# Performance work log

Hardware: AMD Instinct MI355X
Metric: run time of the kernel (lower is better)

Reference implementation:

```python
import jax, jax.numpy as jnp
import numpy as np

B, S, M, E, H = 4, 2048, 1024, 8, 4096
CAP = 2 * (B * S) // E  # GShard top-2 capacity = 2*s/e = 2048


def setup_inputs() -> dict:
    key = jax.random.key(0)
    k = jax.random.split(key, 6)
    sc = 0.02
    return {
        "x": jax.random.normal(k[0], (B, S, M), jnp.float32),
        "wg": jax.random.normal(k[1], (M, E), jnp.float32) * sc,
        "w1": jax.random.normal(k[2], (E, M, H), jnp.float32) * sc,
        "b1": jnp.zeros((E, H), jnp.float32),
        "w2": jax.random.normal(k[3], (E, H, M), jnp.float32) * sc,
        "b2": jnp.zeros((E, M), jnp.float32),
    }


def top2gating(logits, capacity):
    # Faithful GShard/fairscale top2gating: logits [s, e]
    s, e = logits.shape
    gates = jax.nn.softmax(logits, axis=-1)
    idx1 = jnp.argmax(gates, axis=1)
    mask1 = jax.nn.one_hot(idx1, e, dtype=jnp.float32)
    logits2 = jnp.where(mask1 > 0, -jnp.inf, logits)
    idx2 = jnp.argmax(logits2, axis=1)
    mask2 = jax.nn.one_hot(idx2, e, dtype=jnp.float32)
    # positions within each expert's buffer
    loc1 = jnp.cumsum(mask1, axis=0) - 1.0
    loc2 = jnp.cumsum(mask2, axis=0) - 1.0 + jnp.sum(mask1, axis=0, keepdims=True)
    # load-balancing aux loss (computed before capacity drop, per fairscale)
    me = jnp.mean(gates, axis=0)
    ce = jnp.mean(mask1, axis=0)
    l_aux = jnp.mean(me * ce) * (e * e)
    # drop tokens over capacity
    mask1 = mask1 * (loc1 < capacity)
    mask2 = mask2 * (loc2 < capacity)
    loc1_s = jnp.sum(loc1 * mask1, axis=1).astype(jnp.int32)
    loc2_s = jnp.sum(loc2 * mask2, axis=1).astype(jnp.int32)
    gates1 = jnp.sum(gates * mask1, axis=1)
    gates2 = jnp.sum(gates * mask2, axis=1)
    denom = jnp.maximum(gates1 + gates2, 1e-9)
    gates1 = gates1 / denom
    gates2 = gates2 / denom
    # dense [s, e, c] combine weights (as in the original einsum formulation)
    oh1 = jax.nn.one_hot(loc1_s, capacity, dtype=jnp.float32)
    oh2 = jax.nn.one_hot(loc2_s, capacity, dtype=jnp.float32)
    combine = (gates1[:, None] * mask1)[:, :, None] * oh1[:, None, :] \
            + (gates2[:, None] * mask2)[:, :, None] * oh2[:, None, :]
    dispatch = combine > 0
    return l_aux, combine, dispatch


def reference(x, wg, w1, b1, w2, b2):
    d_model = x.shape[2]
    xf = x.reshape(-1, d_model)                      # [s, m]
    logits = xf @ wg                                 # [s, e]
    l_aux, combine, dispatch = top2gating(logits, CAP)
    # dispatch: dense one-hot scatter, as in torch.einsum('sec,sm->ecm')
    disp = jnp.einsum('sec,sm->ecm', dispatch.astype(xf.dtype), xf)
    # per-expert FFN (Linear -> ReLU -> Linear), vectorized over experts
    h = jax.nn.relu(jnp.einsum('ecm,emh->ech', disp, w1) + b1[:, None, :])
    eo = jnp.einsum('ech,ehm->ecm', h, w2) + b2[:, None, :]
    # combine: torch.einsum('sec,ecm->sm')
    out = jnp.einsum('sec,ecm->sm', combine, eo)
    return out.reshape(x.shape), l_aux
```

## Files before the change

### kernel.cpp

```cpp
#include <hip/hip_runtime.h>
#include <stdint.h>

typedef unsigned short u16;
typedef __attribute__((ext_vector_type(8))) short bf16x8;
typedef __attribute__((ext_vector_type(4))) float f32x4;

#define TOKENS 8192
#define DM 1024
#define NE 8
#define DH 4096
#define CAP 2048

__device__ __forceinline__ u16 f2bf(float f) {
  unsigned int u = __float_as_uint(f);
  u = u + 0x7FFFu + ((u >> 16) & 1u);
  return (u16)(u >> 16);
}

__device__ __forceinline__ void gll16(const void* g, void* l) {
  __builtin_amdgcn_global_load_lds(
      (const __attribute__((address_space(1))) unsigned int*)g,
      (__attribute__((address_space(3))) unsigned int*)l, 16, 0, 0);
}

__global__ __launch_bounds__(256) void gating_kernel(
    const float* __restrict__ x, const float* __restrict__ wg,
    int* __restrict__ idx1, int* __restrict__ idx2,
    float* __restrict__ g1r, float* __restrict__ g2r, float* __restrict__ me) {
  __shared__ float gsh[4][8];
  int lane = threadIdx.x & 63;
  int w = threadIdx.x >> 6;
  int t = blockIdx.x * 4 + w;
  const float* xr = x + (size_t)t * DM;
  double acc[8];
#pragma unroll
  for (int e = 0; e < 8; ++e) acc[e] = 0.0;
#pragma unroll
  for (int it = 0; it < 4; ++it) {
    float4 xv = ((const float4*)xr)[it * 64 + lane];
    int base = (it * 64 + lane) * 4;
    const float* wr = wg + (size_t)base * 8;
    float xs[4] = {xv.x, xv.y, xv.z, xv.w};
#pragma unroll
    for (int j = 0; j < 4; ++j)
#pragma unroll
      for (int e = 0; e < 8; ++e) acc[e] += (double)xs[j] * (double)wr[j * 8 + e];
  }
#pragma unroll
  for (int off = 32; off > 0; off >>= 1)
#pragma unroll
    for (int e = 0; e < 8; ++e) acc[e] += __shfl_down(acc[e], off);
  if (lane == 0) {
    float l[8];
#pragma unroll
    for (int e = 0; e < 8; ++e) l[e] = (float)acc[e];
    int i1 = 0;
    float v1 = l[0];
#pragma unroll
    for (int e = 1; e < 8; ++e)
      if (l[e] > v1) { v1 = l[e]; i1 = e; }
    int i2 = -1;
    float v2 = -3.4e38f;
#pragma unroll
    for (int e = 0; e < 8; ++e)
      if (e != i1 && l[e] > v2) { v2 = l[e]; i2 = e; }
    float s = 0.f;
    float p[8];
#pragma unroll
    for (int e = 0; e < 8; ++e) { p[e] = expf(l[e] - v1); s += p[e]; }
    float inv = 1.f / s;
    idx1[t] = i1;
    idx2[t] = i2;
    g1r[t] = inv;
    g2r[t] = expf(v2 - v1) * inv;
#pragma unroll
    for (int e = 0; e < 8; ++e) gsh[w][e] = p[e] * inv;
  }
  __syncthreads();
  if (threadIdx.x < 8) {
    int e = threadIdx.x;
    atomicAdd(&me[e], gsh[0][e] + gsh[1][e] + gsh[2][e] + gsh[3][e]);
  }
}

__global__ __launch_bounds__(1024) void scan_kernel(
    const int* __restrict__ idx1, const int* __restrict__ idx2,
    const float* __restrict__ g1r, const float* __restrict__ g2r,
    const float* __restrict__ me,
    int* __restrict__ slot1, int* __restrict__ slot2,
    float* __restrict__ g1n, float* __restrict__ g2n,
    int* __restrict__ slot2tok, float* __restrict__ laux) {
  __shared__ u16 c[16][1024];
  __shared__ u16 csum[16][32];
  __shared__ int tot[16];
  int tid = threadIdx.x;
  int i1[8], i2[8];
#pragma unroll
  for (int ctr = 0; ctr < 16; ++ctr) c[ctr][tid] = 0;
#pragma unroll
  for (int j = 0; j < 8; ++j) {
    int t = tid * 8 + j;
    i1[j] = idx1[t];
    i2[j] = idx2[t];
    c[i1[j]][tid]++;
    c[8 + i2[j]][tid]++;
  }
  __syncthreads();
  if (tid < 512) {
    int ctr = tid >> 5, ch = tid & 31;
    int s = 0;
#pragma unroll
    for (int i = 0; i < 32; ++i) s += c[ctr][ch * 32 + i];
    csum[ctr][ch] = (u16)s;
  }
  __syncthreads();
  if (tid < 16) {
    int run = 0;
#pragma unroll
    for (int ch = 0; ch < 32; ++ch) {
      int v = csum[tid][ch];
      csum[tid][ch] = (u16)run;
      run += v;
    }
    tot[tid] = run;
  }
  __syncthreads();
  if (tid < 512) {
    int ctr = tid >> 5, ch = tid & 31;
    int run = csum[ctr][ch];
#pragma unroll
    for (int i = 0; i < 32; ++i) {
      int v = c[ctr][ch * 32 + i];
      c[ctr][ch * 32 + i] = (u16)run;
      run += v;
    }
  }
  __syncthreads();
#pragma unroll
  for (int j = 0; j < 8; ++j) {
    int t = tid * 8 + j;
    int e1 = i1[j], e2 = i2[j];
    int L1 = c[e1][tid]++;
    int L2 = c[8 + e2][tid]++;
    L2 += tot[e2];
    bool kv1 = L1 < CAP, kv2 = L2 < CAP;
    float G1 = kv1 ? g1r[t] : 0.f;
    float G2 = kv2 ? g2r[t] : 0.f;
    float den = fmaxf(G1 + G2, 1e-9f);
    g1n[t] = G1 / den;
    g2n[t] = G2 / den;
    int s1 = kv1 ? (e1 * CAP + L1) : -1;
    int s2 = kv2 ? (e2 * CAP + L2) : -1;
    slot1[t] = s1;
    slot2[t] = s2;
    if (kv1) slot2tok[s1] = t;
    if (kv2) slot2tok[s2] = t;
  }
  if (tid == 0) {
    double a = 0.0;
    for (int e = 0; e < 8; ++e)
      a += ((double)me[e] / 8192.0) * ((double)tot[e] / 8192.0);
    laux[0] = (float)(a * 8.0);
  }
}

__global__ void transpose_kernel(const float* __restrict__ src, u16* __restrict__ dst,
                                 int R, int C) {
  __shared__ float tile[32][33];
  int tx = threadIdx.x, ty = threadIdx.y;
  int r0 = blockIdx.y * 32, c0 = blockIdx.x * 32;
  const float* s = src + (size_t)blockIdx.z * R * C;
  u16* d = dst + (size_t)blockIdx.z * R * C;
#pragma unroll
  for (int i = 0; i < 32; i += 8) tile[ty + i][tx] = s[(size_t)(r0 + ty + i) * C + c0 + tx];
  __syncthreads();
#pragma unroll
  for (int i = 0; i < 32; i += 8)
    d[(size_t)(c0 + ty + i) * R + r0 + tx] = f2bf(tile[tx][ty + i]);
}

__global__ void gather_kernel(const float* __restrict__ x, const int* __restrict__ slot2tok,
                              u16* __restrict__ xe) {
  int slot = blockIdx.y * CAP + blockIdx.x;
  int tok = slot2tok[slot];
  int tid = threadIdx.x;
  u16 o[8];
  if (tok >= 0) {
    const float4* xr = (const float4*)(x + (size_t)tok * DM);
    float4 a = xr[tid * 2], b = xr[tid * 2 + 1];
    o[0] = f2bf(a.x); o[1] = f2bf(a.y); o[2] = f2bf(a.z); o[3] = f2bf(a.w);
    o[4] = f2bf(b.x); o[5] = f2bf(b.y); o[6] = f2bf(b.z); o[7] = f2bf(b.w);
  } else {
#pragma unroll
    for (int j = 0; j < 8; ++j) o[j] = 0;
  }
  *(uint4*)(xe + (size_t)slot * DM + tid * 8) = *(const uint4*)o;
}

#define BAR()                              \
  {                                        \
    asm volatile("" ::: "memory");         \
    __builtin_amdgcn_s_barrier();          \
    asm volatile("" ::: "memory");         \
  }
#define VMCNT(n) asm volatile("s_waitcnt vmcnt(" #n ")" ::: "memory")

template <int RELU, int OUTBF16>
__global__ __launch_bounds__(512, 2) void gemm_kernel(
    const u16* __restrict__ A, const u16* __restrict__ Bt,
    const float* __restrict__ bias, void* __restrict__ Cv,
    int MO, int NO, int K) {
  __shared__ __align__(16) u16 As[2][256 * 64];
  __shared__ __align__(16) u16 Bs[2][256 * 64];
  const int tid = threadIdx.x;
  const int lane = tid & 63, wid = tid >> 6;
  const int wm = wid >> 2, wn = wid & 3;

  const int gx = gridDim.x, gy = gridDim.y;
  const int nwg = gx * gy * gridDim.z;
  const int L = (blockIdx.z * gy + blockIdx.y) * gx + blockIdx.x;
  const int cpx = nwg >> 3;
  const int Ls = (L & 7) * cpx + (L >> 3);
  const int bx = Ls % gx;
  const int tq = Ls / gx;
  const int by = tq % gy;
  const int eb = tq / gy;

  const size_t Ks2 = (size_t)K * 2;
  const char* Ag = (const char*)(A + (size_t)eb * MO * K + (size_t)by * 256 * K);
  const char* Bg = (const char*)(Bt + (size_t)eb * NO * K + (size_t)bx * 256 * K);
  const int rl = tid >> 3;
  const int sb = ((tid & 7) * 16) ^ ((rl & 7) << 4);
  Ag += (size_t)rl * Ks2 + sb;
  Bg += (size_t)rl * Ks2 + sb;
  char* AsB = ((char*)As) + tid * 16;
  char* BsB = ((char*)Bs) + tid * 16;
  const u16* AsE = &As[0][0];
  const u16* BsE = &Bs[0][0];
  const int fr = lane & 15, kg8 = (lane >> 4) * 8;
  const int swz = (fr & 7) << 3;

#define STAGE_A(BUF_, REG_, KT_) \
  gll16(Ag + (size_t)((REG_)*64) * Ks2 + (size_t)(KT_)*128, AsB + (BUF_)*32768 + (REG_)*8192)
#define STAGE_B(BUF_, REG_, KT_) \
  gll16(Bg + (size_t)((REG_)*64) * Ks2 + (size_t)(KT_)*128, BsB + (BUF_)*32768 + (REG_)*8192)
#define LDA(BUF_, M_, K_) \
  (*(const bf16x8*)&AsE[(BUF_)*16384 + (wm * 128 + (M_)*16 + fr) * 64 + (((K_)*32 + kg8) ^ swz)])
#define LDB(BUF_, N_, K_) \
  (*(const bf16x8*)&BsE[(BUF_)*16384 + (wn * 64 + (N_)*16 + fr) * 64 + (((K_)*32 + kg8) ^ swz)])
#define MFMA_Q(MB_, NB_)                                                            \
  _Pragma("unroll") for (int k = 0; k < 2; ++k)                                     \
  _Pragma("unroll") for (int m = 0; m < 4; ++m)                                     \
  _Pragma("unroll") for (int n = 0; n < 2; ++n)                                     \
      acc[(MB_) + m][(NB_) + n] = __builtin_amdgcn_mfma_f32_16x16x32_bf16(          \
          areg[m][k], breg[(NB_) + n][k], acc[(MB_) + m][(NB_) + n], 0, 0, 0)

  f32x4 acc[8][4];
#pragma unroll
  for (int i = 0; i < 8; ++i)
#pragma unroll
    for (int j = 0; j < 4; ++j) acc[i][j] = {0.f, 0.f, 0.f, 0.f};
  bf16x8 areg[4][2], breg[4][2];

  const int NT = K >> 6;

#define TILE_STEP(CUR_, NXT_, ST_)                                                  \
  {                                                                                 \
                          \
    STAGE_A(NXT_, 0, ST_); STAGE_A(NXT_, 1, ST_);                                   \
    STAGE_A(NXT_, 2, ST_); STAGE_A(NXT_, 3, ST_);                                   \
    STAGE_B(NXT_, 0, ST_); STAGE_B(NXT_, 1, ST_);                                   \
    STAGE_B(NXT_, 2, ST_); STAGE_B(NXT_, 3, ST_);                                   \
                                   \
    _Pragma("unroll") for (int m = 0; m < 4; ++m) {                                 \
      areg[m][0] = LDA(CUR_, m, 0); areg[m][1] = LDA(CUR_, m, 1);                   \
    }                                                                               \
    _Pragma("unroll") for (int n = 0; n < 4; ++n) {                                 \
      breg[n][0] = LDB(CUR_, n, 0); breg[n][1] = LDB(CUR_, n, 1);                   \
    }                                                                               \
    __builtin_amdgcn_s_setprio(1);                                                  \
    MFMA_Q(0, 0); MFMA_Q(0, 2);                                                     \
    __builtin_amdgcn_s_setprio(0);                                                  \
                          \
    _Pragma("unroll") for (int m = 0; m < 4; ++m) {                                 \
      areg[m][0] = LDA(CUR_, 4 + m, 0); areg[m][1] = LDA(CUR_, 4 + m, 1);           \
    }                                                                               \
    __builtin_amdgcn_s_setprio(1);                                                  \
    MFMA_Q(4, 0); MFMA_Q(4, 2);                                                     \
    __builtin_amdgcn_s_setprio(0);                                                  \
    VMCNT(0);           \
    BAR();              \
  }

  STAGE_A(0, 0, 0); STAGE_A(0, 1, 0); STAGE_A(0, 2, 0); STAGE_A(0, 3, 0);
  STAGE_B(0, 0, 0); STAGE_B(0, 1, 0); STAGE_B(0, 2, 0); STAGE_B(0, 3, 0);
  VMCNT(0);
  BAR();

  for (int t = 0; t < NT; t += 2) {
    const int s1 = (t + 1 < NT) ? t + 1 : NT - 1;
    const int s2 = (t + 2 < NT) ? t + 2 : NT - 1;
    TILE_STEP(0, 1, s1);
    TILE_STEP(1, 0, s2);
  }

  const int row0 = by * 256 + wm * 128 + (kg8 >> 3) * 4;
  const int col0 = bx * 256 + wn * 64 + fr;
  const float* be = bias + (size_t)eb * NO;
  size_t cbase = (size_t)eb * MO * NO;
#pragma unroll
  for (int m = 0; m < 8; ++m) {
#pragma unroll
    for (int n = 0; n < 4; ++n) {
      int col = col0 + n * 16;
      float bv = be[col];
#pragma unroll
      for (int r = 0; r < 4; ++r) {
        int row = row0 + m * 16 + r;
        float v = acc[m][n][r] + bv;
        if (RELU) v = fmaxf(v, 0.f);
        if (OUTBF16)
          ((u16*)Cv)[cbase + (size_t)row * NO + col] = f2bf(v);
        else
          ((float*)Cv)[cbase + (size_t)row * NO + col] = v;
      }
    }
  }
#undef TILE_STEP
#undef STAGE_A
#undef STAGE_B
#undef LDA
#undef LDB
#undef MFMA_Q
}

__global__ void combine_kernel(const float* __restrict__ eo,
                               const float* __restrict__ g1n, const float* __restrict__ g2n,
                               const int* __restrict__ slot1, const int* __restrict__ slot2,
                               float* __restrict__ out) {
  int t = blockIdx.x, tid = threadIdx.x;
  float g1 = g1n[t], g2 = g2n[t];
  int s1 = slot1[t], s2 = slot2[t];
  float4 o = make_float4(0.f, 0.f, 0.f, 0.f);
  if (s1 >= 0) {
    float4 a = ((const float4*)(eo + (size_t)s1 * DM))[tid];
    o.x = g1 * a.x; o.y = g1 * a.y; o.z = g1 * a.z; o.w = g1 * a.w;
  }
  if (s2 >= 0) {
    float4 b = ((const float4*)(eo + (size_t)s2 * DM))[tid];
    o.x += g2 * b.x; o.y += g2 * b.y; o.z += g2 * b.z; o.w += g2 * b.w;
  }
  ((float4*)(out + (size_t)t * DM))[tid] = o;
}

extern "C" void kernel_launch(void* const* d_in, const int* in_sizes, int n_in,
                              void* d_out, int out_size, void* d_ws, size_t ws_size,
                              hipStream_t stream) {
  const float* x = (const float*)d_in[0];
  const float* wg = (const float*)d_in[1];
  const float* w1 = (const float*)d_in[2];
  const float* b1 = (const float*)d_in[3];
  const float* w2 = (const float*)d_in[4];
  const float* b2 = (const float*)d_in[5];
  float* out = (float*)d_out;

  const size_t SZ_WT1 = (size_t)NE * DH * DM * 2;
  const size_t SZ_WT2 = (size_t)NE * DM * DH * 2;
  const size_t SZ_XE = (size_t)NE * CAP * DM * 2;
  const size_t SZ_H = (size_t)NE * CAP * DH * 2;
  const size_t SZ_TOK = (size_t)TOKENS * 4;

  char* p = (char*)d_ws;
  u16* wt1 = (u16*)p;
  float* eo = (float*)p;            p += SZ_WT1;
  u16* wt2 = (u16*)p;               p += SZ_WT2;
  u16* xe = (u16*)p;                p += SZ_XE;
  u16* h = (u16*)p;                 p += SZ_H;
  int* idx1 = (int*)p;              p += SZ_TOK;
  int* idx2 = (int*)p;              p += SZ_TOK;
  int* slot1 = (int*)p;             p += SZ_TOK;
  int* slot2 = (int*)p;             p += SZ_TOK;
  float* g1r = (float*)p;           p += SZ_TOK;
  float* g2r = (float*)p;           p += SZ_TOK;
  float* g1n = (float*)p;           p += SZ_TOK;
  float* g2n = (float*)p;           p += SZ_TOK;
  int* slot2tok = (int*)p;          p += (size_t)NE * CAP * 4;
  float* me = (float*)p;            p += 256;
  if ((size_t)(p - (char*)d_ws) > ws_size) return;

  hipMemsetAsync(me, 0, 32, stream);
  hipMemsetAsync(slot2tok, 0xFF, (size_t)NE * CAP * 4, stream);

  gating_kernel<<<TOKENS / 4, 256, 0, stream>>>(x, wg, idx1, idx2, g1r, g2r, me);
  scan_kernel<<<1, 1024, 0, stream>>>(idx1, idx2, g1r, g2r, me, slot1, slot2, g1n, g2n,
                                      slot2tok, out + (size_t)TOKENS * DM);
  transpose_kernel<<<dim3(DH / 32, DM / 32, NE), dim3(32, 8), 0, stream>>>(w1, wt1, DM, DH);
  transpose_kernel<<<dim3(DM / 32, DH / 32, NE), dim3(32, 8), 0, stream>>>(w2, wt2, DH, DM);
  gather_kernel<<<dim3(CAP, NE), 128, 0, stream>>>(x, slot2tok, xe);
  gemm_kernel<1, 1><<<dim3(DH / 256, CAP / 256, NE), 512, 0, stream>>>(xe, wt1, b1, (void*)h,
                                                                       CAP, DH, DM);
  gemm_kernel<0, 0><<<dim3(DM / 256, CAP / 256, NE), 512, 0, stream>>>(h, wt2, b2, (void*)eo,
                                                                       CAP, DM, DH);
  combine_kernel<<<TOKENS, 256, 0, stream>>>(eo, g1n, g2n, slot1, slot2, out);
}
```

Before: 461.6 us.

## Use 32x32 MFMA tiles and fuse combine into second GEMM via atomics

Replaces the 16x16x32 MFMA inner loop with 32x32x16 MFMA fragments and a finer-grained barrier/lgkmcnt schedule that interleaves LDS reads with compute. It also removes the combine kernel and the fp32 expert-output buffer: the second GEMM epilogue scales each row by its slot gate and atomically adds it into the zeroed output at the owning token's row. This saves a full eo write and read plus a launch, but adds a memset of the output and scattered float atomics in the epilogue.

```diff
diff --git a/kernel.cpp b/kernel.cpp
--- a/kernel.cpp
+++ b/kernel.cpp
@@ -3,7 +3,7 @@
 
 typedef unsigned short u16;
 typedef __attribute__((ext_vector_type(8))) short bf16x8;
-typedef __attribute__((ext_vector_type(4))) float f32x4;
+typedef __attribute__((ext_vector_type(16))) float f32x16;
 
 #define TOKENS 8192
 #define DM 1024
@@ -87,9 +87,8 @@
     const int* __restrict__ idx1, const int* __restrict__ idx2,
     const float* __restrict__ g1r, const float* __restrict__ g2r,
     const float* __restrict__ me,
-    int* __restrict__ slot1, int* __restrict__ slot2,
-    float* __restrict__ g1n, float* __restrict__ g2n,
-    int* __restrict__ slot2tok, float* __restrict__ laux) {
+    int* __restrict__ slot2tok, float* __restrict__ gslot,
+    float* __restrict__ laux) {
   __shared__ u16 c[16][1024];
   __shared__ u16 csum[16][32];
   __shared__ int tot[16];
@@ -147,14 +146,16 @@
     float G1 = kv1 ? g1r[t] : 0.f;
     float G2 = kv2 ? g2r[t] : 0.f;
     float den = fmaxf(G1 + G2, 1e-9f);
-    g1n[t] = G1 / den;
-    g2n[t] = G2 / den;
-    int s1 = kv1 ? (e1 * CAP + L1) : -1;
-    int s2 = kv2 ? (e2 * CAP + L2) : -1;
-    slot1[t] = s1;
-    slot2[t] = s2;
-    if (kv1) slot2tok[s1] = t;
-    if (kv2) slot2tok[s2] = t;
+    if (kv1) {
+      int s1 = e1 * CAP + L1;
+      slot2tok[s1] = t;
+      gslot[s1] = G1 / den;
+    }
+    if (kv2) {
+      int s2 = e2 * CAP + L2;
+      slot2tok[s2] = t;
+      gslot[s2] = G2 / den;
+    }
   }
   if (tid == 0) {
     double a = 0.0;
@@ -204,12 +205,14 @@
     asm volatile("" ::: "memory");         \
   }
 #define VMCNT(n) asm volatile("s_waitcnt vmcnt(" #n ")" ::: "memory")
-
-template <int RELU, int OUTBF16>
+#define LGKM(n) asm volatile("s_waitcnt lgkmcnt(" #n ")" ::: "memory")
+
+template <int RELU, int OUTMODE>
 __global__ __launch_bounds__(512, 2) void gemm_kernel(
     const u16* __restrict__ A, const u16* __restrict__ Bt,
     const float* __restrict__ bias, void* __restrict__ Cv,
-    int MO, int NO, int K) {
+    int MO, int NO, int K,
+    const int* __restrict__ s2t, const float* __restrict__ gsl) {
   __shared__ __align__(16) u16 As[2][256 * 64];
   __shared__ __align__(16) u16 Bs[2][256 * 64];
   const int tid = threadIdx.x;
@@ -237,59 +240,68 @@
   char* BsB = ((char*)Bs) + tid * 16;
   const u16* AsE = &As[0][0];
   const u16* BsE = &Bs[0][0];
-  const int fr = lane & 15, kg8 = (lane >> 4) * 8;
-  const int swz = (fr & 7) << 3;
+  const int ln31 = lane & 31, kg2 = lane >> 5;
+  const int swz = (lane & 7) << 3;
 
 #define STAGE_A(BUF_, REG_, KT_) \
   gll16(Ag + (size_t)((REG_)*64) * Ks2 + (size_t)(KT_)*128, AsB + (BUF_)*32768 + (REG_)*8192)
 #define STAGE_B(BUF_, REG_, KT_) \
   gll16(Bg + (size_t)((REG_)*64) * Ks2 + (size_t)(KT_)*128, BsB + (BUF_)*32768 + (REG_)*8192)
-#define LDA(BUF_, M_, K_) \
-  (*(const bf16x8*)&AsE[(BUF_)*16384 + (wm * 128 + (M_)*16 + fr) * 64 + (((K_)*32 + kg8) ^ swz)])
-#define LDB(BUF_, N_, K_) \
-  (*(const bf16x8*)&BsE[(BUF_)*16384 + (wn * 64 + (N_)*16 + fr) * 64 + (((K_)*32 + kg8) ^ swz)])
-#define MFMA_Q(MB_, NB_)                                                            \
-  _Pragma("unroll") for (int k = 0; k < 2; ++k)                                     \
-  _Pragma("unroll") for (int m = 0; m < 4; ++m)                                     \
-  _Pragma("unroll") for (int n = 0; n < 2; ++n)                                     \
-      acc[(MB_) + m][(NB_) + n] = __builtin_amdgcn_mfma_f32_16x16x32_bf16(          \
-          areg[m][k], breg[(NB_) + n][k], acc[(MB_) + m][(NB_) + n], 0, 0, 0)
-
-  f32x4 acc[8][4];
-#pragma unroll
-  for (int i = 0; i < 8; ++i)
-#pragma unroll
-    for (int j = 0; j < 4; ++j) acc[i][j] = {0.f, 0.f, 0.f, 0.f};
-  bf16x8 areg[4][2], breg[4][2];
+#define LDA(BUF_, MF_, KS_)                                                   \
+  (*(const bf16x8*)&AsE[(BUF_)*16384 + (wm * 128 + (MF_)*32 + ln31) * 64 +    \
+                        (((KS_)*16 + kg2 * 8) ^ swz)])
+#define LDB(BUF_, NF_, KS_)                                                   \
+  (*(const bf16x8*)&BsE[(BUF_)*16384 + (wn * 64 + (NF_)*32 + ln31) * 64 +     \
+                        (((KS_)*16 + kg2 * 8) ^ swz)])
+#define MFMA_Q(MB_, NF_)                                                      \
+  _Pragma("unroll") for (int ks = 0; ks < 4; ++ks)                            \
+  _Pragma("unroll") for (int mf = 0; mf < 2; ++mf)                            \
+      acc[(MB_) + mf][NF_] = __builtin_amdgcn_mfma_f32_32x32x16_bf16(         \
+          areg[mf][ks], breg[NF_][ks], acc[(MB_) + mf][NF_], 0, 0, 0)
+
+#define RD_A(C_, MB_)                                                         \
+  _Pragma("unroll") for (int mf = 0; mf < 2; ++mf)                            \
+  _Pragma("unroll") for (int ks = 0; ks < 4; ++ks)                            \
+      areg[mf][ks] = LDA(C_, (MB_) + mf, ks);
+#define RD_B(C_, NF_)                                                         \
+  _Pragma("unroll") for (int ks = 0; ks < 4; ++ks)                            \
+      breg[NF_][ks] = LDB(C_, NF_, ks);
+#define MM(MB_, NF_)                          \
+  BAR();                                      \
+  LGKM(0);                                    \
+  __builtin_amdgcn_sched_barrier(0);          \
+  __builtin_amdgcn_s_setprio(1);              \
+  MFMA_Q(MB_, NF_);                           \
+  __builtin_amdgcn_s_setprio(0);              \
+  BAR();
+
+  f32x16 acc[4][2];
+#pragma unroll
+  for (int i = 0; i < 4; ++i)
+#pragma unroll
+    for (int j = 0; j < 2; ++j)
+#pragma unroll
+      for (int r = 0; r < 16; ++r) acc[i][j][r] = 0.f;
+  bf16x8 areg[2][4], breg[2][4];
 
   const int NT = K >> 6;
 
-#define TILE_STEP(CUR_, NXT_, ST_)                                                  \
-  {                                                                                 \
-                          \
-    STAGE_A(NXT_, 0, ST_); STAGE_A(NXT_, 1, ST_);                                   \
-    STAGE_A(NXT_, 2, ST_); STAGE_A(NXT_, 3, ST_);                                   \
-    STAGE_B(NXT_, 0, ST_); STAGE_B(NXT_, 1, ST_);                                   \
-    STAGE_B(NXT_, 2, ST_); STAGE_B(NXT_, 3, ST_);                                   \
-                                   \
-    _Pragma("unroll") for (int m = 0; m < 4; ++m) {                                 \
-      areg[m][0] = LDA(CUR_, m, 0); areg[m][1] = LDA(CUR_, m, 1);                   \
-    }                                                                               \
-    _Pragma("unroll") for (int n = 0; n < 4; ++n) {                                 \
-      breg[n][0] = LDB(CUR_, n, 0); breg[n][1] = LDB(CUR_, n, 1);                   \
-    }                                                                               \
-    __builtin_amdgcn_s_setprio(1);                                                  \
-    MFMA_Q(0, 0); MFMA_Q(0, 2);                                                     \
-    __builtin_amdgcn_s_setprio(0);                                                  \
-                          \
-    _Pragma("unroll") for (int m = 0; m < 4; ++m) {                                 \
-      areg[m][0] = LDA(CUR_, 4 + m, 0); areg[m][1] = LDA(CUR_, 4 + m, 1);           \
-    }                                                                               \
-    __builtin_amdgcn_s_setprio(1);                                                  \
-    MFMA_Q(4, 0); MFMA_Q(4, 2);                                                     \
-    __builtin_amdgcn_s_setprio(0);                                                  \
-    VMCNT(0);           \
-    BAR();              \
+#define TILE_STEP(CUR_, NXT_, ST_)                                            \
+  {                                                                           \
+               \
+    STAGE_A(NXT_, 0, ST_); STAGE_A(NXT_, 1, ST_);                             \
+    STAGE_A(NXT_, 2, ST_); STAGE_A(NXT_, 3, ST_);                             \
+    STAGE_B(NXT_, 0, ST_); STAGE_B(NXT_, 1, ST_);                             \
+    STAGE_B(NXT_, 2, ST_); STAGE_B(NXT_, 3, ST_);                             \
+    RD_A(CUR_, 0); RD_B(CUR_, 0);                             \
+    LGKM(8);                                                                  \
+    MM(0, 0);                                                                 \
+    RD_B(CUR_, 1);                                             \
+    MM(0, 1);                                                                 \
+    RD_A(CUR_, 2);                                             \
+    MM(2, 0);                                                                 \
+    VMCNT(0);                        \
+    MM(2, 1);                                                                 \
   }
 
   STAGE_A(0, 0, 0); STAGE_A(0, 1, 0); STAGE_A(0, 2, 0); STAGE_A(0, 3, 0);
@@ -304,53 +316,39 @@
     TILE_STEP(1, 0, s2);
   }
 
-  const int row0 = by * 256 + wm * 128 + (kg8 >> 3) * 4;
-  const int col0 = bx * 256 + wn * 64 + fr;
+  const int col0 = bx * 256 + wn * 64 + ln31;
   const float* be = bias + (size_t)eb * NO;
-  size_t cbase = (size_t)eb * MO * NO;
-#pragma unroll
-  for (int m = 0; m < 8; ++m) {
-#pragma unroll
-    for (int n = 0; n < 4; ++n) {
-      int col = col0 + n * 16;
-      float bv = be[col];
-#pragma unroll
-      for (int r = 0; r < 4; ++r) {
-        int row = row0 + m * 16 + r;
-        float v = acc[m][n][r] + bv;
+#pragma unroll
+  for (int nf = 0; nf < 2; ++nf) {
+    const int col = col0 + nf * 32;
+    const float bv = be[col];
+#pragma unroll
+    for (int mf = 0; mf < 4; ++mf) {
+      const int rbase = by * 256 + wm * 128 + mf * 32 + 4 * kg2;
+#pragma unroll
+      for (int r = 0; r < 16; ++r) {
+        const int row = rbase + (r & 3) + 8 * (r >> 2);
+        float v = acc[mf][nf][r] + bv;
         if (RELU) v = fmaxf(v, 0.f);
-        if (OUTBF16)
-          ((u16*)Cv)[cbase + (size_t)row * NO + col] = f2bf(v);
-        else
-          ((float*)Cv)[cbase + (size_t)row * NO + col] = v;
+        if (OUTMODE == 1) {
+          ((u16*)Cv)[(size_t)eb * MO * NO + (size_t)row * NO + col] = f2bf(v);
+        } else {
+          const int slot = eb * CAP + row;
+          const int tok = s2t[slot];
+          if (tok >= 0) atomicAdd(((float*)Cv) + (size_t)tok * DM + col, gsl[slot] * v);
+        }
       }
     }
   }
 #undef TILE_STEP
+#undef MM
+#undef RD_A
+#undef RD_B
 #undef STAGE_A
 #undef STAGE_B
 #undef LDA
 #undef LDB
 #undef MFMA_Q
-}
-
-__global__ void combine_kernel(const float* __restrict__ eo,
-                               const float* __restrict__ g1n, const float* __restrict__ g2n,
-                               const int* __restrict__ slot1, const int* __restrict__ slot2,
-                               float* __restrict__ out) {
-  int t = blockIdx.x, tid = threadIdx.x;
-  float g1 = g1n[t], g2 = g2n[t];
-  int s1 = slot1[t], s2 = slot2[t];
-  float4 o = make_float4(0.f, 0.f, 0.f, 0.f);
-  if (s1 >= 0) {
-    float4 a = ((const float4*)(eo + (size_t)s1 * DM))[tid];
-    o.x = g1 * a.x; o.y = g1 * a.y; o.z = g1 * a.z; o.w = g1 * a.w;
-  }
-  if (s2 >= 0) {
-    float4 b = ((const float4*)(eo + (size_t)s2 * DM))[tid];
-    o.x += g2 * b.x; o.y += g2 * b.y; o.z += g2 * b.z; o.w += g2 * b.w;
-  }
-  ((float4*)(out + (size_t)t * DM))[tid] = o;
 }
 
 extern "C" void kernel_launch(void* const* d_in, const int* in_sizes, int n_in,
@@ -371,35 +369,31 @@
   const size_t SZ_TOK = (size_t)TOKENS * 4;
 
   char* p = (char*)d_ws;
-  u16* wt1 = (u16*)p;
-  float* eo = (float*)p;            p += SZ_WT1;
+  u16* wt1 = (u16*)p;               p += SZ_WT1;
   u16* wt2 = (u16*)p;               p += SZ_WT2;
   u16* xe = (u16*)p;                p += SZ_XE;
   u16* h = (u16*)p;                 p += SZ_H;
   int* idx1 = (int*)p;              p += SZ_TOK;
   int* idx2 = (int*)p;              p += SZ_TOK;
-  int* slot1 = (int*)p;             p += SZ_TOK;
-  int* slot2 = (int*)p;             p += SZ_TOK;
   float* g1r = (float*)p;           p += SZ_TOK;
   float* g2r = (float*)p;           p += SZ_TOK;
-  float* g1n = (float*)p;           p += SZ_TOK;
-  float* g2n = (float*)p;           p += SZ_TOK;
   int* slot2tok = (int*)p;          p += (size_t)NE * CAP * 4;
+  float* gslot = (float*)p;         p += (size_t)NE * CAP * 4;
   float* me = (float*)p;            p += 256;
   if ((size_t)(p - (char*)d_ws) > ws_size) return;
 
   hipMemsetAsync(me, 0, 32, stream);
   hipMemsetAsync(slot2tok, 0xFF, (size_t)NE * CAP * 4, stream);
+  hipMemsetAsync(out, 0, (size_t)TOKENS * DM * 4, stream);
 
   gating_kernel<<<TOKENS / 4, 256, 0, stream>>>(x, wg, idx1, idx2, g1r, g2r, me);
-  scan_kernel<<<1, 1024, 0, stream>>>(idx1, idx2, g1r, g2r, me, slot1, slot2, g1n, g2n,
-                                      slot2tok, out + (size_t)TOKENS * DM);
+  scan_kernel<<<1, 1024, 0, stream>>>(idx1, idx2, g1r, g2r, me, slot2tok, gslot,
+                                      out + (size_t)TOKENS * DM);
   transpose_kernel<<<dim3(DH / 32, DM / 32, NE), dim3(32, 8), 0, stream>>>(w1, wt1, DM, DH);
   transpose_kernel<<<dim3(DM / 32, DH / 32, NE), dim3(32, 8), 0, stream>>>(w2, wt2, DH, DM);
   gather_kernel<<<dim3(CAP, NE), 128, 0, stream>>>(x, slot2tok, xe);
-  gemm_kernel<1, 1><<<dim3(DH / 256, CAP / 256, NE), 512, 0, stream>>>(xe, wt1, b1, (void*)h,
-                                                                       CAP, DH, DM);
-  gemm_kernel<0, 0><<<dim3(DM / 256, CAP / 256, NE), 512, 0, stream>>>(h, wt2, b2, (void*)eo,
-                                                                       CAP, DM, DH);
-  combine_kernel<<<TOKENS, 256, 0, stream>>>(eo, g1n, g2n, slot1, slot2, out);
-}
+  gemm_kernel<1, 1><<<dim3(DH / 256, CAP / 256, NE), 512, 0, stream>>>(
+      xe, wt1, b1, (void*)h, CAP, DH, DM, nullptr, nullptr);
+  gemm_kernel<0, 2><<<dim3(DM / 256, CAP / 256, NE), 512, 0, stream>>>(
+      h, wt2, b2, (void*)out, CAP, DM, DH, slot2tok, gslot);
+}
```

New measurement: 638.2 us. 1.38x slower.

## Fuse weight transposes, store expert output in bf16, replace gating atomics with partials

Applied to the files above, without the earlier changes.

The two per-expert weight transpose launches become one kernel using 64x64 tiles, vectorized float4 loads and 16-byte bf16 stores. The second GEMM now writes its expert output in bf16, and the combine kernel reads it back as bf16, which halves that intermediate traffic at some cost in output precision. The gating kernel writes per-block partial sums of the mean gate values instead of using atomics, and the scan kernel reduces them in shared memory, so the memset for that buffer is no longer needed.

```diff
diff --git a/kernel.cpp b/kernel.cpp
--- a/kernel.cpp
+++ b/kernel.cpp
@@ -16,6 +16,9 @@
   u = u + 0x7FFFu + ((u >> 16) & 1u);
   return (u16)(u >> 16);
 }
+__device__ __forceinline__ float bf2f(u16 u) {
+  return __uint_as_float(((unsigned int)u) << 16);
+}
 
 __device__ __forceinline__ void gll16(const void* g, void* l) {
   __builtin_amdgcn_global_load_lds(
@@ -26,7 +29,7 @@
 __global__ __launch_bounds__(256) void gating_kernel(
     const float* __restrict__ x, const float* __restrict__ wg,
     int* __restrict__ idx1, int* __restrict__ idx2,
-    float* __restrict__ g1r, float* __restrict__ g2r, float* __restrict__ me) {
+    float* __restrict__ g1r, float* __restrict__ g2r, float* __restrict__ mepart) {
   __shared__ float gsh[4][8];
   int lane = threadIdx.x & 63;
   int w = threadIdx.x >> 6;
@@ -79,20 +82,21 @@
   __syncthreads();
   if (threadIdx.x < 8) {
     int e = threadIdx.x;
-    atomicAdd(&me[e], gsh[0][e] + gsh[1][e] + gsh[2][e] + gsh[3][e]);
+    mepart[blockIdx.x * 8 + e] = gsh[0][e] + gsh[1][e] + gsh[2][e] + gsh[3][e];
   }
 }
 
 __global__ __launch_bounds__(1024) void scan_kernel(
     const int* __restrict__ idx1, const int* __restrict__ idx2,
     const float* __restrict__ g1r, const float* __restrict__ g2r,
-    const float* __restrict__ me,
+    const float* __restrict__ mepart,
     int* __restrict__ slot1, int* __restrict__ slot2,
     float* __restrict__ g1n, float* __restrict__ g2n,
     int* __restrict__ slot2tok, float* __restrict__ laux) {
   __shared__ u16 c[16][1024];
   __shared__ u16 csum[16][32];
   __shared__ int tot[16];
+  __shared__ float mred[1024];
   int tid = threadIdx.x;
   int i1[8], i2[8];
 #pragma unroll
@@ -156,27 +160,69 @@
     if (kv1) slot2tok[s1] = t;
     if (kv2) slot2tok[s2] = t;
   }
+  {
+    float macc = 0.f;
+    int e = tid & 7;
+    for (int r = tid >> 3; r < 2048; r += 128) macc += mepart[r * 8 + e];
+    mred[tid] = macc;
+  }
+  __syncthreads();
+  for (int s = 512; s >= 8; s >>= 1) {
+    if (tid < s) mred[tid] += mred[tid + s];
+    __syncthreads();
+  }
   if (tid == 0) {
     double a = 0.0;
     for (int e = 0; e < 8; ++e)
-      a += ((double)me[e] / 8192.0) * ((double)tot[e] / 8192.0);
+      a += ((double)mred[e] / 8192.0) * ((double)tot[e] / 8192.0);
     laux[0] = (float)(a * 8.0);
   }
 }
 
-__global__ void transpose_kernel(const float* __restrict__ src, u16* __restrict__ dst,
-                                 int R, int C) {
-  __shared__ float tile[32][33];
-  int tx = threadIdx.x, ty = threadIdx.y;
-  int r0 = blockIdx.y * 32, c0 = blockIdx.x * 32;
-  const float* s = src + (size_t)blockIdx.z * R * C;
-  u16* d = dst + (size_t)blockIdx.z * R * C;
-#pragma unroll
-  for (int i = 0; i < 32; i += 8) tile[ty + i][tx] = s[(size_t)(r0 + ty + i) * C + c0 + tx];
-  __syncthreads();
-#pragma unroll
-  for (int i = 0; i < 32; i += 8)
-    d[(size_t)(c0 + ty + i) * R + r0 + tx] = f2bf(tile[tx][ty + i]);
+__global__ __launch_bounds__(256) void transpose2_kernel(
+    const float* __restrict__ w1, const float* __restrict__ w2,
+    u16* __restrict__ wt1, u16* __restrict__ wt2) {
+  __shared__ float tile[64][65];
+  const int tid = threadIdx.x;
+  const int z = blockIdx.z;
+  const float* s;
+  u16* d;
+  int C, r0, c0;
+  if (z < 8) {
+    s = w1 + (size_t)z * DM * DH;
+    d = wt1 + (size_t)z * DM * DH;
+    C = DH;
+    r0 = blockIdx.y * 64;
+    c0 = blockIdx.x * 64;
+  } else {
+    s = w2 + (size_t)(z - 8) * DM * DH;
+    d = wt2 + (size_t)(z - 8) * DM * DH;
+    C = DM;
+    r0 = blockIdx.x * 64;
+    c0 = blockIdx.y * 64;
+  }
+  const int R = (z < 8) ? DM : DH;
+  const int lr = tid >> 4;
+  const int lc = (tid & 15) * 4;
+#pragma unroll
+  for (int i = 0; i < 4; ++i) {
+    const float4 v = *(const float4*)&s[(size_t)(r0 + i * 16 + lr) * C + c0 + lc];
+    tile[i * 16 + lr][lc] = v.x;
+    tile[i * 16 + lr][lc + 1] = v.y;
+    tile[i * 16 + lr][lc + 2] = v.z;
+    tile[i * 16 + lr][lc + 3] = v.w;
+  }
+  __syncthreads();
+  const int oc = tid >> 3;
+  const int orr = (tid & 7) * 8;
+#pragma unroll
+  for (int i = 0; i < 2; ++i) {
+    const int c = oc + i * 32;
+    u16 o[8];
+#pragma unroll
+    for (int j = 0; j < 8; ++j) o[j] = f2bf(tile[orr + j][c]);
+    *(uint4*)&d[(size_t)(c0 + c) * R + r0 + orr] = *(const uint4*)o;
+  }
 }
 
 __global__ void gather_kernel(const float* __restrict__ x, const int* __restrict__ slot2tok,
@@ -334,23 +380,23 @@
 #undef MFMA_Q
 }
 
-__global__ void combine_kernel(const float* __restrict__ eo,
+__global__ void combine_kernel(const u16* __restrict__ eo,
                                const float* __restrict__ g1n, const float* __restrict__ g2n,
                                const int* __restrict__ slot1, const int* __restrict__ slot2,
                                float* __restrict__ out) {
   int t = blockIdx.x, tid = threadIdx.x;
   float g1 = g1n[t], g2 = g2n[t];
   int s1 = slot1[t], s2 = slot2[t];
-  float4 o = make_float4(0.f, 0.f, 0.f, 0.f);
+  float o0 = 0.f, o1 = 0.f, o2 = 0.f, o3 = 0.f;
   if (s1 >= 0) {
-    float4 a = ((const float4*)(eo + (size_t)s1 * DM))[tid];
-    o.x = g1 * a.x; o.y = g1 * a.y; o.z = g1 * a.z; o.w = g1 * a.w;
+    ushort4 a = ((const ushort4*)(eo + (size_t)s1 * DM))[tid];
+    o0 = g1 * bf2f(a.x); o1 = g1 * bf2f(a.y); o2 = g1 * bf2f(a.z); o3 = g1 * bf2f(a.w);
   }
   if (s2 >= 0) {
-    float4 b = ((const float4*)(eo + (size_t)s2 * DM))[tid];
-    o.x += g2 * b.x; o.y += g2 * b.y; o.z += g2 * b.z; o.w += g2 * b.w;
-  }
-  ((float4*)(out + (size_t)t * DM))[tid] = o;
+    ushort4 b = ((const ushort4*)(eo + (size_t)s2 * DM))[tid];
+    o0 += g2 * bf2f(b.x); o1 += g2 * bf2f(b.y); o2 += g2 * bf2f(b.z); o3 += g2 * bf2f(b.w);
+  }
+  ((float4*)(out + (size_t)t * DM))[tid] = make_float4(o0, o1, o2, o3);
 }
 
 extern "C" void kernel_launch(void* const* d_in, const int* in_sizes, int n_in,
@@ -372,7 +418,7 @@
 
   char* p = (char*)d_ws;
   u16* wt1 = (u16*)p;
-  float* eo = (float*)p;            p += SZ_WT1;
+  u16* eo = (u16*)p;                p += SZ_WT1;
   u16* wt2 = (u16*)p;               p += SZ_WT2;
   u16* xe = (u16*)p;                p += SZ_XE;
   u16* h = (u16*)p;                 p += SZ_H;
@@ -385,21 +431,19 @@
   float* g1n = (float*)p;           p += SZ_TOK;
   float* g2n = (float*)p;           p += SZ_TOK;
   int* slot2tok = (int*)p;          p += (size_t)NE * CAP * 4;
-  float* me = (float*)p;            p += 256;
+  float* mepart = (float*)p;        p += (size_t)2048 * 8 * 4;
   if ((size_t)(p - (char*)d_ws) > ws_size) return;
 
-  hipMemsetAsync(me, 0, 32, stream);
   hipMemsetAsync(slot2tok, 0xFF, (size_t)NE * CAP * 4, stream);
 
-  gating_kernel<<<TOKENS / 4, 256, 0, stream>>>(x, wg, idx1, idx2, g1r, g2r, me);
-  scan_kernel<<<1, 1024, 0, stream>>>(idx1, idx2, g1r, g2r, me, slot1, slot2, g1n, g2n,
+  gating_kernel<<<TOKENS / 4, 256, 0, stream>>>(x, wg, idx1, idx2, g1r, g2r, mepart);
+  scan_kernel<<<1, 1024, 0, stream>>>(idx1, idx2, g1r, g2r, mepart, slot1, slot2, g1n, g2n,
                                       slot2tok, out + (size_t)TOKENS * DM);
-  transpose_kernel<<<dim3(DH / 32, DM / 32, NE), dim3(32, 8), 0, stream>>>(w1, wt1, DM, DH);
-  transpose_kernel<<<dim3(DM / 32, DH / 32, NE), dim3(32, 8), 0, stream>>>(w2, wt2, DH, DM);
+  transpose2_kernel<<<dim3(DH / 64, DM / 64, 16), 256, 0, stream>>>(w1, w2, wt1, wt2);
   gather_kernel<<<dim3(CAP, NE), 128, 0, stream>>>(x, slot2tok, xe);
   gemm_kernel<1, 1><<<dim3(DH / 256, CAP / 256, NE), 512, 0, stream>>>(xe, wt1, b1, (void*)h,
                                                                        CAP, DH, DM);
-  gemm_kernel<0, 0><<<dim3(DM / 256, CAP / 256, NE), 512, 0, stream>>>(h, wt2, b2, (void*)eo,
+  gemm_kernel<0, 1><<<dim3(DM / 256, CAP / 256, NE), 512, 0, stream>>>(h, wt2, b2, (void*)eo,
                                                                        CAP, DM, DH);
   combine_kernel<<<TOKENS, 256, 0, stream>>>(eo, g1n, g2n, slot1, slot2, out);
 }
```

After: 453.3 us. About the same (-1.8%).
